# Optimization experiments

Hardware: AMD Instinct MI355X
Metric: run time of the kernel (lower is better)

The kernel has to match this reference:

```python
import jax, jax.numpy as jnp
import numpy as np

NUM_PARTS = 10
COS_W = 10.0
COS_K = 100.0
EPS = 1e-6

B, V, F, VHD = 512, 6890, 13776, 20000


def setup_inputs() -> dict:
    key = jax.random.key(0)
    k1, k2, k3, k4, k5 = jax.random.split(key, 5)
    vertices = jax.random.normal(k1, (B, V, 3), dtype=jnp.float32)
    bary = jax.random.uniform(k2, (VHD, 3), dtype=jnp.float32)
    faces = jax.random.randint(k3, (F, 3), 0, V)
    hd_fid = jax.random.randint(k4, (VHD,), 0, F)
    part_fid = jax.random.randint(k5, (F,), 0, NUM_PARTS)
    return {"vertices": vertices, "bary": bary, "faces": faces,
            "hd_fid": hd_fid, "part_fid": part_fid}


def reference(vertices, bary, faces, hd_fid, part_fid):
    # --- per-part mesh volume (signed tetra volumes, segment-summed by part) ---
    tri = vertices[:, faces]                       # [B, F, 3, 3] gather face corners
    t0, t1, t2 = tri[:, :, 0], tri[:, :, 1], tri[:, :, 2]
    vol_f = jnp.einsum('bfi,bfi->bf', jnp.cross(t0, t1), t2) / 6.0   # [B, F]
    fid_onehot = jax.nn.one_hot(part_fid, NUM_PARTS, dtype=vertices.dtype)  # [F, P]
    per_part_volume = vol_f @ fid_onehot           # [B, P]

    # --- HDfy: barycentric sampling of HD vertices on faces ---
    w = bary / jnp.sum(bary, axis=-1, keepdims=True)          # barycentric weights [VHD,3]
    vidx = faces[hd_fid]                                       # [VHD, 3]
    hd_corners = vertices[:, vidx]                             # [B, VHD, 3, 3]
    vertices_hd = jnp.einsum('bvkd,vk->bvd', hd_corners, w)    # [B, VHD, 3]

    # --- per-HD-vertex part volume (bmm with one-hot == gather) ---
    hd_part = part_fid[hd_fid]                                 # [VHD]
    vol_hd = per_part_volume[:, hd_part]                       # [B, VHD]

    # --- center of mass ---
    com = jnp.sum(vertices_hd * vol_hd[..., None], axis=1) / jnp.sum(vol_hd, axis=1, keepdims=True)  # [B,3]

    # --- center of pressure via height-based pressure weights ---
    h = vertices_hd[:, :, 1]                                   # [B, VHD], ground plane at y=0
    inside = (h < 0.0).astype(vertices_hd.dtype)
    outside = (h >= 0.0).astype(vertices_hd.dtype)
    pw = inside * (1.0 - COS_K * h) + outside * jnp.exp(-COS_W * h)
    cop = jnp.sum(vertices_hd * pw[..., None], axis=1) / (jnp.sum(pw, axis=1, keepdims=True) + EPS)  # [B,3]

    # --- stability loss: xz distance between COM and COP ---
    d = com - cop
    return jnp.sqrt(d[:, 0] ** 2 + d[:, 2] ** 2)               # [B]
```

## Files before the change

kernel.cpp:

```cpp
#include <hip/hip_runtime.h>
#include <math.h>

#define NB     512
#define NV     6890
#define NF     13776
#define NVHD   20000
#define NPARTS 10
#define NTHREADS 1024
#define NWAVES (NTHREADS/64)
#define CUT    6697
#define NCHF   ((NF + 63) / 64)
#define NCHH   ((NVHD + 63) / 64)

__global__ void build_tables(const float* __restrict__ bary,
                             const int*   __restrict__ faces,
                             const int*   __restrict__ hd_fid,
                             const int*   __restrict__ part_fid,
                             uint2* __restrict__ f_pack,
                             uint4* __restrict__ hd_pack)
{
    int i = blockIdx.x * blockDim.x + threadIdx.x;
    if (i < NF) {
        f_pack[i] = make_uint2((unsigned)faces[3*i+0] | ((unsigned)faces[3*i+1] << 16),
                               (unsigned)faces[3*i+2] | ((unsigned)part_fid[i]  << 16));
    }
    if (i < NVHD) {
        int fid = hd_fid[i];
        float b0 = bary[3*i+0], b1 = bary[3*i+1], b2 = bary[3*i+2];
        float inv = 1.0f / (b0 + b1 + b2);
        hd_pack[i] = make_uint4((unsigned)faces[3*fid+0] | ((unsigned)faces[3*fid+1] << 16),
                                (unsigned)faces[3*fid+2] | ((unsigned)part_fid[fid] << 16),
                                __float_as_uint(b0*inv), __float_as_uint(b1*inv));
    }
}

__global__ __launch_bounds__(1024) void split_overflow(
    uint2* __restrict__ f_pack, uint4* __restrict__ hd_pack,
    uint2* __restrict__ ovf_f,  uint4* __restrict__ ovf_h,
    int*   __restrict__ counts)
{
    __shared__ int cnt[NCHH];
    const int tid = threadIdx.x, wave = tid >> 6, lane = tid & 63;
    const unsigned long long lowmask = (1ull << lane) - 1ull;

    if (blockIdx.x == 0) {
        for (int c = wave; c < NCHF; c += NWAVES) {
            int i = c * 64 + lane;
            bool bad = false;
            if (i < NF) {
                uint2 ft = f_pack[i];
                bad = ((ft.x & 0xFFFFu) >= CUT) || ((ft.x >> 16) >= CUT) || ((ft.y & 0xFFFFu) >= CUT);
            }
            unsigned long long m = __ballot(bad);
            if (lane == 0) cnt[c] = (int)__popcll(m);
        }
        __syncthreads();
        if (wave == 0) {
            int carry = 0;
            #pragma unroll
            for (int seg = 0; seg < (NCHF + 63) / 64; seg++) {
                int idx = seg * 64 + lane;
                int v = (idx < NCHF) ? cnt[idx] : 0;
                int incl = v;
                #pragma unroll
                for (int off = 1; off < 64; off <<= 1) { int n = __shfl_up(incl, off, 64); if (lane >= off) incl += n; }
                if (idx < NCHF) cnt[idx] = incl - v + carry;
                carry += __shfl(incl, 63, 64);
            }
            if (lane == 0) counts[0] = carry;
        }
        __syncthreads();
        for (int c = wave; c < NCHF; c += NWAVES) {
            int i = c * 64 + lane;
            bool valid = i < NF;
            uint2 ft = valid ? f_pack[i] : make_uint2(0u, 0u);
            bool bad = valid && (((ft.x & 0xFFFFu) >= CUT) || ((ft.x >> 16) >= CUT) || ((ft.y & 0xFFFFu) >= CUT));
            unsigned long long m = __ballot(bad);
            if (bad) {
                int rank = (int)__popcll(m & lowmask);
                ovf_f[cnt[c] + rank] = ft;
                f_pack[i] = make_uint2((unsigned)CUT | ((unsigned)CUT << 16), (unsigned)CUT);
            }
        }
    } else {
        for (int c = wave; c < NCHH; c += NWAVES) {
            int i = c * 64 + lane;
            bool bad = false;
            if (i < NVHD) {
                uint4 hp = hd_pack[i];
                bad = ((hp.x & 0xFFFFu) >= CUT) || ((hp.x >> 16) >= CUT) || ((hp.y & 0xFFFFu) >= CUT);
            }
            unsigned long long m = __ballot(bad);
            if (lane == 0) cnt[c] = (int)__popcll(m);
        }
        __syncthreads();
        if (wave == 0) {
            int carry = 0;
            #pragma unroll
            for (int seg = 0; seg < (NCHH + 63) / 64; seg++) {
                int idx = seg * 64 + lane;
                int v = (idx < NCHH) ? cnt[idx] : 0;
                int incl = v;
                #pragma unroll
                for (int off = 1; off < 64; off <<= 1) { int n = __shfl_up(incl, off, 64); if (lane >= off) incl += n; }
                if (idx < NCHH) cnt[idx] = incl - v + carry;
                carry += __shfl(incl, 63, 64);
            }
            if (lane == 0) counts[1] = carry;
        }
        __syncthreads();
        for (int c = wave; c < NCHH; c += NWAVES) {
            int i = c * 64 + lane;
            bool valid = i < NVHD;
            uint4 hp = valid ? hd_pack[i] : make_uint4(0u, 0u, 0u, 0u);
            bool bad = valid && (((hp.x & 0xFFFFu) >= CUT) || ((hp.x >> 16) >= CUT) || ((hp.y & 0xFFFFu) >= CUT));
            unsigned long long m = __ballot(bad);
            if (bad) {
                int rank = (int)__popcll(m & lowmask);
                ovf_h[cnt[c] + rank] = hp;
                hd_pack[i] = make_uint4((unsigned)CUT | ((unsigned)CUT << 16),
                                        (unsigned)CUT | ((unsigned)NPARTS << 16),
                                        0u, 0u);
            }
        }
    }
}

__global__ __launch_bounds__(NTHREADS, 8) void stab_kernel(
    const float* __restrict__ vertices,
    const uint2* __restrict__ f_pack,
    const uint4* __restrict__ hd_pack,
    const uint2* __restrict__ ovf_f,
    const uint4* __restrict__ ovf_h,
    const int*   __restrict__ counts,
    float*       __restrict__ out)
{
    __shared__ float2 sxy[CUT + 1];
    __shared__ float  szz[CUT + 1];
    __shared__ float  spart[NPARTS + 1];
    __shared__ float  sredp[NWAVES][NPARTS];

    const int tid  = threadIdx.x;
    const int b    = blockIdx.x;
    const int wave = tid >> 6;
    const int lane = tid & 63;
    const float* __restrict__ vb = vertices + (size_t)b * (NV * 3);

    for (int v = tid; v < CUT; v += NTHREADS) {
        float x = vb[3 * v + 0];
        float y = vb[3 * v + 1];
        float z = vb[3 * v + 2];
        sxy[v] = make_float2(x, y);
        szz[v] = z;
    }
    if (tid == 0) { sxy[CUT] = make_float2(0.f, 100.f); szz[CUT] = 0.f; }
    __syncthreads();

    float accp[NPARTS];
    #pragma unroll
    for (int q = 0; q < NPARTS; q++) accp[q] = 0.f;

    #pragma unroll 2
    for (int f = tid; f < NF; f += NTHREADS) {
        uint2 ft = f_pack[f];
        int i0 = ft.x & 0xFFFF, i1 = ft.x >> 16;
        int i2 = ft.y & 0xFFFF, p  = (int)(ft.y >> 16);
        float2 t0 = sxy[i0]; float z0 = szz[i0];
        float2 t1 = sxy[i1]; float z1 = szz[i1];
        float2 t2 = sxy[i2]; float z2 = szz[i2];
        float cx = t0.y * z1   - z0   * t1.y;
        float cy = z0   * t1.x - t0.x * z1;
        float cz = t0.x * t1.y - t0.y * t1.x;
        float vol = (cx * t2.x + cy * t2.y + cz * z2) * (1.0f / 6.0f);
        #pragma unroll
        for (int q = 0; q < NPARTS; q++) accp[q] += (p == q) ? vol : 0.f;
    }

    const int nofF = counts[0];
    for (int k = tid; k < nofF; k += NTHREADS) {
        uint2 ft = ovf_f[k];
        int i0 = ft.x & 0xFFFF, i1 = ft.x >> 16;
        int i2 = ft.y & 0xFFFF, p  = (int)(ft.y >> 16);
        float x0 = vb[3*i0+0], y0 = vb[3*i0+1], z0 = vb[3*i0+2];
        float x1 = vb[3*i1+0], y1 = vb[3*i1+1], z1 = vb[3*i1+2];
        float x2 = vb[3*i2+0], y2 = vb[3*i2+1], z2 = vb[3*i2+2];
        float cx = y0 * z1 - z0 * y1;
        float cy = z0 * x1 - x0 * z1;
        float cz = x0 * y1 - y0 * x1;
        float vol = (cx * x2 + cy * y2 + cz * z2) * (1.0f / 6.0f);
        #pragma unroll
        for (int q = 0; q < NPARTS; q++) accp[q] += (p == q) ? vol : 0.f;
    }

    #pragma unroll
    for (int q = 0; q < NPARTS; q++) {
        float s = accp[q];
        #pragma unroll
        for (int off = 32; off > 0; off >>= 1) s += __shfl_down(s, off, 64);
        accp[q] = s;
    }
    if (lane == 0) {
        #pragma unroll
        for (int q = 0; q < NPARTS; q++) sredp[wave][q] = accp[q];
    }
    __syncthreads();
    if (tid < NPARTS) {
        float s = 0.f;
        #pragma unroll
        for (int w = 0; w < NWAVES; w++) s += sredp[w][tid];
        spart[tid] = s;
    }
    if (tid == NPARTS) spart[NPARTS] = 0.f;
    __syncthreads();

    float sVx = 0.f, sVz = 0.f, sVol = 0.f;
    float sPx = 0.f, sPz = 0.f, sPw  = 0.f;

    #pragma unroll 2
    for (int v = tid; v < NVHD; v += NTHREADS) {
        uint4 hp = hd_pack[v];
        int i0 = hp.x & 0xFFFF, i1 = hp.x >> 16;
        int i2 = hp.y & 0xFFFF, p  = (int)(hp.y >> 16);
        float w0 = __uint_as_float(hp.z);
        float w1 = __uint_as_float(hp.w);
        float w2 = 1.0f - w0 - w1;
        float2 t0 = sxy[i0]; float z0 = szz[i0];
        float2 t1 = sxy[i1]; float z1 = szz[i1];
        float2 t2 = sxy[i2]; float z2 = szz[i2];
        float x = w0 * t0.x + w1 * t1.x + w2 * t2.x;
        float y = w0 * t0.y + w1 * t1.y + w2 * t2.y;
        float z = w0 * z0   + w1 * z1   + w2 * z2;
        float vol = spart[p];
        float pw  = (y < 0.f) ? fmaf(-100.f, y, 1.f) : __expf(-10.f * y);
        sVx += x * vol;  sVz += z * vol;  sVol += vol;
        sPx += x * pw;   sPz += z * pw;   sPw  += pw;
    }

    const int nofH = counts[1];
    for (int k = tid; k < nofH; k += NTHREADS) {
        uint4 hp = ovf_h[k];
        int i0 = hp.x & 0xFFFF, i1 = hp.x >> 16;
        int i2 = hp.y & 0xFFFF, p  = (int)(hp.y >> 16);
        float w0 = __uint_as_float(hp.z);
        float w1 = __uint_as_float(hp.w);
        float w2 = 1.0f - w0 - w1;
        float x0 = vb[3*i0+0], y0 = vb[3*i0+1], z0 = vb[3*i0+2];
        float x1 = vb[3*i1+0], y1 = vb[3*i1+1], z1 = vb[3*i1+2];
        float x2 = vb[3*i2+0], y2 = vb[3*i2+1], z2 = vb[3*i2+2];
        float x = w0 * x0 + w1 * x1 + w2 * x2;
        float y = w0 * y0 + w1 * y1 + w2 * y2;
        float z = w0 * z0 + w1 * z1 + w2 * z2;
        float vol = spart[p];
        float pw  = (y < 0.f) ? fmaf(-100.f, y, 1.f) : __expf(-10.f * y);
        sVx += x * vol;  sVz += z * vol;  sVol += vol;
        sPx += x * pw;   sPz += z * pw;   sPw  += pw;
    }

    float vals[6] = {sVx, sVz, sVol, sPx, sPz, sPw};
    #pragma unroll
    for (int q = 0; q < 6; q++) {
        float s = vals[q];
        #pragma unroll
        for (int off = 32; off > 0; off >>= 1) s += __shfl_down(s, off, 64);
        vals[q] = s;
    }
    float* sred6 = &sredp[0][0];
    if (lane == 0) {
        #pragma unroll
        for (int q = 0; q < 6; q++) sred6[wave * 6 + q] = vals[q];
    }
    __syncthreads();
    if (tid == 0) {
        float r[6];
        #pragma unroll
        for (int q = 0; q < 6; q++) {
            float s = 0.f;
            #pragma unroll
            for (int w = 0; w < NWAVES; w++) s += sred6[w * 6 + q];
            r[q] = s;
        }
        float invVol = 1.0f / r[2];
        float invPw  = 1.0f / (r[5] + 1e-6f);
        float comx = r[0] * invVol, comz = r[1] * invVol;
        float copx = r[3] * invPw,  copz = r[4] * invPw;
        float d0 = comx - copx, d2 = comz - copz;
        out[b] = sqrtf(d0 * d0 + d2 * d2);
    }
}

extern "C" void kernel_launch(void* const* d_in, const int* in_sizes, int n_in,
                              void* d_out, int out_size, void* d_ws, size_t ws_size,
                              hipStream_t stream) {
    const float* vertices = (const float*)d_in[0];
    const float* bary     = (const float*)d_in[1];
    const int*   faces    = (const int*)d_in[2];
    const int*   hd_fid   = (const int*)d_in[3];
    const int*   part_fid = (const int*)d_in[4];
    float* out = (float*)d_out;

    char* ws = (char*)d_ws;
    uint2* f_pack  = (uint2*)ws;
    uint4* hd_pack = (uint4*)(ws + 110208);
    uint4* ovf_h   = (uint4*)(ws + 110208 + 320000);
    uint2* ovf_f   = (uint2*)(ws + 110208 + 640000);
    int*   counts  = (int*)(ws + 110208 + 640000 + 110208);

    build_tables<<<(NVHD + 255) / 256, 256, 0, stream>>>(bary, faces, hd_fid, part_fid,
                                                         f_pack, hd_pack);
    split_overflow<<<2, 1024, 0, stream>>>(f_pack, hd_pack, ovf_f, ovf_h, counts);
    stab_kernel<<<NB, NTHREADS, 0, stream>>>(vertices, f_pack, hd_pack, ovf_f, ovf_h, counts, out);
}
```

Before: 65.69 us.

## Fuse table build into overflow split and precompute per-part HD counts

Merges the build_tables and split_overflow kernels into a single two-block prep kernel that builds the packed tables directly from the raw inputs, removing one kernel launch and a write-then-reread of the packed tables. The HD block also counts how many HD vertices belong to each part. The main kernel then gets the total volume as the sum over parts of part volume times count, instead of accumulating and reducing a per-vertex volume sum. In exchange, the two-block prep kernel now does all table construction serially with very little parallelism, so its own runtime may grow.

```diff
diff --git a/kernel.cpp b/kernel.cpp
--- a/kernel.cpp
+++ b/kernel.cpp
@@ -12,34 +12,19 @@
 #define NCHF   ((NF + 63) / 64)
 #define NCHH   ((NVHD + 63) / 64)
 
-__global__ void build_tables(const float* __restrict__ bary,
-                             const int*   __restrict__ faces,
-                             const int*   __restrict__ hd_fid,
-                             const int*   __restrict__ part_fid,
-                             uint2* __restrict__ f_pack,
-                             uint4* __restrict__ hd_pack)
-{
-    int i = blockIdx.x * blockDim.x + threadIdx.x;
-    if (i < NF) {
-        f_pack[i] = make_uint2((unsigned)faces[3*i+0] | ((unsigned)faces[3*i+1] << 16),
-                               (unsigned)faces[3*i+2] | ((unsigned)part_fid[i]  << 16));
-    }
-    if (i < NVHD) {
-        int fid = hd_fid[i];
-        float b0 = bary[3*i+0], b1 = bary[3*i+1], b2 = bary[3*i+2];
-        float inv = 1.0f / (b0 + b1 + b2);
-        hd_pack[i] = make_uint4((unsigned)faces[3*fid+0] | ((unsigned)faces[3*fid+1] << 16),
-                                (unsigned)faces[3*fid+2] | ((unsigned)part_fid[fid] << 16),
-                                __float_as_uint(b0*inv), __float_as_uint(b1*inv));
-    }
-}
-
-__global__ __launch_bounds__(1024) void split_overflow(
-    uint2* __restrict__ f_pack, uint4* __restrict__ hd_pack,
-    uint2* __restrict__ ovf_f,  uint4* __restrict__ ovf_h,
+__global__ __launch_bounds__(1024) void prep(
+    const float* __restrict__ bary,
+    const int*   __restrict__ faces,
+    const int*   __restrict__ hd_fid,
+    const int*   __restrict__ part_fid,
+    uint2* __restrict__ f_pack,
+    uint4* __restrict__ hd_pack,
+    uint2* __restrict__ ovf_f,
+    uint4* __restrict__ ovf_h,
     int*   __restrict__ counts)
 {
     __shared__ int cnt[NCHH];
+    __shared__ int snp[NWAVES][NPARTS];
     const int tid = threadIdx.x, wave = tid >> 6, lane = tid & 63;
     const unsigned long long lowmask = (1ull << lane) - 1ull;
 
@@ -48,8 +33,8 @@
             int i = c * 64 + lane;
             bool bad = false;
             if (i < NF) {
-                uint2 ft = f_pack[i];
-                bad = ((ft.x & 0xFFFFu) >= CUT) || ((ft.x >> 16) >= CUT) || ((ft.y & 0xFFFFu) >= CUT);
+                int i0 = faces[3*i+0], i1 = faces[3*i+1], i2 = faces[3*i+2];
+                bad = (i0 >= CUT) || (i1 >= CUT) || (i2 >= CUT);
             }
             unsigned long long m = __ballot(bad);
             if (lane == 0) cnt[c] = (int)__popcll(m);
@@ -73,22 +58,40 @@
         for (int c = wave; c < NCHF; c += NWAVES) {
             int i = c * 64 + lane;
             bool valid = i < NF;
-            uint2 ft = valid ? f_pack[i] : make_uint2(0u, 0u);
-            bool bad = valid && (((ft.x & 0xFFFFu) >= CUT) || ((ft.x >> 16) >= CUT) || ((ft.y & 0xFFFFu) >= CUT));
+            uint2 ft = make_uint2(0u, 0u);
+            bool bad = false;
+            if (valid) {
+                int i0 = faces[3*i+0], i1 = faces[3*i+1], i2 = faces[3*i+2];
+                ft = make_uint2((unsigned)i0 | ((unsigned)i1 << 16),
+                                (unsigned)i2 | ((unsigned)part_fid[i] << 16));
+                bad = (i0 >= CUT) || (i1 >= CUT) || (i2 >= CUT);
+            }
             unsigned long long m = __ballot(bad);
-            if (bad) {
-                int rank = (int)__popcll(m & lowmask);
-                ovf_f[cnt[c] + rank] = ft;
-                f_pack[i] = make_uint2((unsigned)CUT | ((unsigned)CUT << 16), (unsigned)CUT);
+            if (valid) {
+                if (bad) {
+                    int rank = (int)__popcll(m & lowmask);
+                    ovf_f[cnt[c] + rank] = ft;
+                    f_pack[i] = make_uint2((unsigned)CUT | ((unsigned)CUT << 16), (unsigned)CUT);
+                } else {
+                    f_pack[i] = ft;
+                }
             }
         }
     } else {
+        int np[NPARTS];
+        #pragma unroll
+        for (int q = 0; q < NPARTS; q++) np[q] = 0;
+
         for (int c = wave; c < NCHH; c += NWAVES) {
             int i = c * 64 + lane;
             bool bad = false;
             if (i < NVHD) {
-                uint4 hp = hd_pack[i];
-                bad = ((hp.x & 0xFFFFu) >= CUT) || ((hp.x >> 16) >= CUT) || ((hp.y & 0xFFFFu) >= CUT);
+                int fid = hd_fid[i];
+                int i0 = faces[3*fid+0], i1 = faces[3*fid+1], i2 = faces[3*fid+2];
+                int p  = part_fid[fid];
+                #pragma unroll
+                for (int q = 0; q < NPARTS; q++) np[q] += (p == q) ? 1 : 0;
+                bad = (i0 >= CUT) || (i1 >= CUT) || (i2 >= CUT);
             }
             unsigned long long m = __ballot(bad);
             if (lane == 0) cnt[c] = (int)__popcll(m);
@@ -112,16 +115,48 @@
         for (int c = wave; c < NCHH; c += NWAVES) {
             int i = c * 64 + lane;
             bool valid = i < NVHD;
-            uint4 hp = valid ? hd_pack[i] : make_uint4(0u, 0u, 0u, 0u);
-            bool bad = valid && (((hp.x & 0xFFFFu) >= CUT) || ((hp.x >> 16) >= CUT) || ((hp.y & 0xFFFFu) >= CUT));
+            uint4 hp = make_uint4(0u, 0u, 0u, 0u);
+            bool bad = false;
+            if (valid) {
+                int fid = hd_fid[i];
+                int i0 = faces[3*fid+0], i1 = faces[3*fid+1], i2 = faces[3*fid+2];
+                float b0 = bary[3*i+0], b1 = bary[3*i+1], b2 = bary[3*i+2];
+                float inv = 1.0f / (b0 + b1 + b2);
+                hp = make_uint4((unsigned)i0 | ((unsigned)i1 << 16),
+                                (unsigned)i2 | ((unsigned)part_fid[fid] << 16),
+                                __float_as_uint(b0*inv), __float_as_uint(b1*inv));
+                bad = (i0 >= CUT) || (i1 >= CUT) || (i2 >= CUT);
+            }
             unsigned long long m = __ballot(bad);
-            if (bad) {
-                int rank = (int)__popcll(m & lowmask);
-                ovf_h[cnt[c] + rank] = hp;
-                hd_pack[i] = make_uint4((unsigned)CUT | ((unsigned)CUT << 16),
-                                        (unsigned)CUT | ((unsigned)NPARTS << 16),
-                                        0u, 0u);
-            }
+            if (valid) {
+                if (bad) {
+                    int rank = (int)__popcll(m & lowmask);
+                    ovf_h[cnt[c] + rank] = hp;
+                    hd_pack[i] = make_uint4((unsigned)CUT | ((unsigned)CUT << 16),
+                                            (unsigned)CUT | ((unsigned)NPARTS << 16),
+                                            0u, 0u);
+                } else {
+                    hd_pack[i] = hp;
+                }
+            }
+        }
+        #pragma unroll
+        for (int q = 0; q < NPARTS; q++) {
+            int s = np[q];
+            #pragma unroll
+            for (int off = 32; off > 0; off >>= 1) s += __shfl_down(s, off, 64);
+            np[q] = s;
+        }
+        if (lane == 0) {
+            #pragma unroll
+            for (int q = 0; q < NPARTS; q++) snp[wave][q] = np[q];
+        }
+        __syncthreads();
+        if (tid < NPARTS) {
+            int s = 0;
+            #pragma unroll
+            for (int w = 0; w < NWAVES; w++) s += snp[w][tid];
+            counts[2 + tid] = s;
         }
     }
 }
@@ -213,8 +248,8 @@
     if (tid == NPARTS) spart[NPARTS] = 0.f;
     __syncthreads();
 
-    float sVx = 0.f, sVz = 0.f, sVol = 0.f;
-    float sPx = 0.f, sPz = 0.f, sPw  = 0.f;
+    float sVx = 0.f, sVz = 0.f;
+    float sPx = 0.f, sPz = 0.f, sPw = 0.f;
 
     #pragma unroll 2
     for (int v = tid; v < NVHD; v += NTHREADS) {
@@ -232,8 +267,8 @@
         float z = w0 * z0   + w1 * z1   + w2 * z2;
         float vol = spart[p];
         float pw  = (y < 0.f) ? fmaf(-100.f, y, 1.f) : __expf(-10.f * y);
-        sVx += x * vol;  sVz += z * vol;  sVol += vol;
-        sPx += x * pw;   sPz += z * pw;   sPw  += pw;
+        sVx += x * vol;  sVz += z * vol;
+        sPx += x * pw;   sPz += z * pw;   sPw += pw;
     }
 
     const int nofH = counts[1];
@@ -252,37 +287,40 @@
         float z = w0 * z0 + w1 * z1 + w2 * z2;
         float vol = spart[p];
         float pw  = (y < 0.f) ? fmaf(-100.f, y, 1.f) : __expf(-10.f * y);
-        sVx += x * vol;  sVz += z * vol;  sVol += vol;
-        sPx += x * pw;   sPz += z * pw;   sPw  += pw;
-    }
-
-    float vals[6] = {sVx, sVz, sVol, sPx, sPz, sPw};
+        sVx += x * vol;  sVz += z * vol;
+        sPx += x * pw;   sPz += z * pw;   sPw += pw;
+    }
+
+    float vals[5] = {sVx, sVz, sPx, sPz, sPw};
     #pragma unroll
-    for (int q = 0; q < 6; q++) {
+    for (int q = 0; q < 5; q++) {
         float s = vals[q];
         #pragma unroll
         for (int off = 32; off > 0; off >>= 1) s += __shfl_down(s, off, 64);
         vals[q] = s;
     }
-    float* sred6 = &sredp[0][0];
+    float* sred5 = &sredp[0][0];
     if (lane == 0) {
         #pragma unroll
-        for (int q = 0; q < 6; q++) sred6[wave * 6 + q] = vals[q];
+        for (int q = 0; q < 5; q++) sred5[wave * 5 + q] = vals[q];
     }
     __syncthreads();
     if (tid == 0) {
-        float r[6];
-        #pragma unroll
-        for (int q = 0; q < 6; q++) {
+        float r[5];
+        #pragma unroll
+        for (int q = 0; q < 5; q++) {
             float s = 0.f;
             #pragma unroll
-            for (int w = 0; w < NWAVES; w++) s += sred6[w * 6 + q];
+            for (int w = 0; w < NWAVES; w++) s += sred5[w * 5 + q];
             r[q] = s;
         }
-        float invVol = 1.0f / r[2];
-        float invPw  = 1.0f / (r[5] + 1e-6f);
+        float sVol = 0.f;
+        #pragma unroll
+        for (int q = 0; q < NPARTS; q++) sVol += spart[q] * (float)counts[2 + q];
+        float invVol = 1.0f / sVol;
+        float invPw  = 1.0f / (r[4] + 1e-6f);
         float comx = r[0] * invVol, comz = r[1] * invVol;
-        float copx = r[3] * invPw,  copz = r[4] * invPw;
+        float copx = r[2] * invPw,  copz = r[3] * invPw;
         float d0 = comx - copx, d2 = comz - copz;
         out[b] = sqrtf(d0 * d0 + d2 * d2);
     }
@@ -305,8 +343,7 @@
     uint2* ovf_f   = (uint2*)(ws + 110208 + 640000);
     int*   counts  = (int*)(ws + 110208 + 640000 + 110208);
 
-    build_tables<<<(NVHD + 255) / 256, 256, 0, stream>>>(bary, faces, hd_fid, part_fid,
-                                                         f_pack, hd_pack);
-    split_overflow<<<2, 1024, 0, stream>>>(f_pack, hd_pack, ovf_f, ovf_h, counts);
+    prep<<<2, 1024, 0, stream>>>(bary, faces, hd_fid, part_fid,
+                                 f_pack, hd_pack, ovf_f, ovf_h, counts);
     stab_kernel<<<NB, NTHREADS, 0, stream>>>(vertices, f_pack, hd_pack, ovf_f, ovf_h, counts, out);
 }
```

New measurement: 108.2 us. +64.7%, slower.

## Sort faces by part and HD vertices by overflow via parallel count/scan/scatter

Applied to the files above, without the earlier changes.

Replaces the pack-then-split preprocessing with a three-kernel counting sort that groups faces by part id (overflow faces last) and HD vertices into clean and overflow segments. The main kernel then sums volumes per part with a plain scalar accumulator instead of a ten-way predicated update per face, and no longer needs sentinel entries or separate overflow arrays. The preprocessing now runs across many blocks rather than two single blocks, at the cost of an extra kernel launch. The per-part loops have data-dependent bounds, so lanes within a wave may diverge at the segment boundaries.

```diff
diff --git a/kernel.cpp b/kernel.cpp
--- a/kernel.cpp
+++ b/kernel.cpp
@@ -11,116 +11,147 @@
 #define CUT    6697
 #define NCHF   ((NF + 63) / 64)
 #define NCHH   ((NVHD + 63) / 64)
-
-__global__ void build_tables(const float* __restrict__ bary,
-                             const int*   __restrict__ faces,
-                             const int*   __restrict__ hd_fid,
-                             const int*   __restrict__ part_fid,
-                             uint2* __restrict__ f_pack,
-                             uint4* __restrict__ hd_pack)
+#define FBLK   ((NF + 255) / 256)
+#define HBLK   ((NVHD + 255) / 256)
+
+__global__ __launch_bounds__(256) void count_kernel(
+    const int* __restrict__ faces, const int* __restrict__ part_fid,
+    const int* __restrict__ hd_fid,
+    int* __restrict__ cntF,
+    int* __restrict__ cntH)
 {
-    int i = blockIdx.x * blockDim.x + threadIdx.x;
-    if (i < NF) {
-        f_pack[i] = make_uint2((unsigned)faces[3*i+0] | ((unsigned)faces[3*i+1] << 16),
-                               (unsigned)faces[3*i+2] | ((unsigned)part_fid[i]  << 16));
-    }
-    if (i < NVHD) {
-        int fid = hd_fid[i];
-        float b0 = bary[3*i+0], b1 = bary[3*i+1], b2 = bary[3*i+2];
-        float inv = 1.0f / (b0 + b1 + b2);
-        hd_pack[i] = make_uint4((unsigned)faces[3*fid+0] | ((unsigned)faces[3*fid+1] << 16),
-                                (unsigned)faces[3*fid+2] | ((unsigned)part_fid[fid] << 16),
+    const int wv = threadIdx.x >> 6, lane = threadIdx.x & 63;
+    if (blockIdx.x < FBLK) {
+        int c = blockIdx.x * 4 + wv;
+        int i = c * 64 + lane;
+        int key = -1;
+        if (i < NF) {
+            int i0 = faces[3*i+0], i1 = faces[3*i+1], i2 = faces[3*i+2];
+            bool bad = (i0 >= CUT) || (i1 >= CUT) || (i2 >= CUT);
+            key = bad ? 10 : part_fid[i];
+        }
+        #pragma unroll
+        for (int q = 0; q < 11; q++) {
+            unsigned long long m = __ballot(key == q);
+            if (lane == 0) cntF[q * NCHF + c] = (int)__popcll(m);
+        }
+    } else {
+        int c = (blockIdx.x - FBLK) * 4 + wv;
+        if (c < NCHH) {
+            int i = c * 64 + lane;
+            int key = -1;
+            if (i < NVHD) {
+                int fid = hd_fid[i];
+                int i0 = faces[3*fid+0], i1 = faces[3*fid+1], i2 = faces[3*fid+2];
+                key = ((i0 >= CUT) || (i1 >= CUT) || (i2 >= CUT)) ? 1 : 0;
+            }
+            #pragma unroll
+            for (int q = 0; q < 2; q++) {
+                unsigned long long m = __ballot(key == q);
+                if (lane == 0) cntH[q * NCHH + c] = (int)__popcll(m);
+            }
+        }
+    }
+}
+
+__global__ __launch_bounds__(1024) void scan_kernel(
+    int* __restrict__ cntF, int* __restrict__ cntH, int* __restrict__ offs)
+{
+    __shared__ int rowtot[13];
+    const int wv = threadIdx.x >> 6, lane = threadIdx.x & 63;
+    if (wv < 11) {
+        int* row = cntF + wv * NCHF;
+        int carry = 0;
+        #pragma unroll
+        for (int seg = 0; seg < (NCHF + 63) / 64; seg++) {
+            int idx = seg * 64 + lane;
+            int v = (idx < NCHF) ? row[idx] : 0;
+            int incl = v;
+            #pragma unroll
+            for (int off = 1; off < 64; off <<= 1) { int n = __shfl_up(incl, off, 64); if (lane >= off) incl += n; }
+            if (idx < NCHF) row[idx] = incl - v + carry;
+            carry += __shfl(incl, 63, 64);
+        }
+        if (lane == 0) rowtot[wv] = carry;
+    } else if (wv < 13) {
+        int r = wv - 11;
+        int* row = cntH + r * NCHH;
+        int carry = 0;
+        #pragma unroll
+        for (int seg = 0; seg < (NCHH + 63) / 64; seg++) {
+            int idx = seg * 64 + lane;
+            int v = (idx < NCHH) ? row[idx] : 0;
+            int incl = v;
+            #pragma unroll
+            for (int off = 1; off < 64; off <<= 1) { int n = __shfl_up(incl, off, 64); if (lane >= off) incl += n; }
+            if (idx < NCHH) row[idx] = incl - v + carry;
+            carry += __shfl(incl, 63, 64);
+        }
+        if (lane == 0) rowtot[11 + r] = carry;
+    }
+    __syncthreads();
+    if (threadIdx.x == 0) {
+        int r = 0;
+        #pragma unroll
+        for (int q = 0; q < 11; q++) { offs[q] = r; r += rowtot[q]; }
+        offs[11] = r;
+        offs[12] = 0;
+        offs[13] = rowtot[11];
+        offs[14] = rowtot[11] + rowtot[12];
+    }
+}
+
+__global__ __launch_bounds__(256) void scatter_kernel(
+    const float* __restrict__ bary, const int* __restrict__ faces,
+    const int* __restrict__ hd_fid, const int* __restrict__ part_fid,
+    const int* __restrict__ cntF, const int* __restrict__ cntH,
+    const int* __restrict__ offs,
+    uint2* __restrict__ f_sorted, uint4* __restrict__ hd_sorted)
+{
+    const int wv = threadIdx.x >> 6, lane = threadIdx.x & 63;
+    const unsigned long long low = (1ull << lane) - 1ull;
+    if (blockIdx.x < FBLK) {
+        int c = blockIdx.x * 4 + wv;
+        int i = c * 64 + lane;
+        int key = -1; uint2 ft = make_uint2(0u, 0u);
+        if (i < NF) {
+            int i0 = faces[3*i+0], i1 = faces[3*i+1], i2 = faces[3*i+2];
+            int p  = part_fid[i];
+            bool bad = (i0 >= CUT) || (i1 >= CUT) || (i2 >= CUT);
+            key = bad ? 10 : p;
+            ft = make_uint2((unsigned)i0 | ((unsigned)i1 << 16),
+                            (unsigned)i2 | ((unsigned)p  << 16));
+        }
+        #pragma unroll
+        for (int q = 0; q < 11; q++) {
+            unsigned long long m = __ballot(key == q);
+            if (key == q) {
+                int rank = (int)__popcll(m & low);
+                f_sorted[offs[q] + cntF[q * NCHF + c] + rank] = ft;
+            }
+        }
+    } else {
+        int c = (blockIdx.x - FBLK) * 4 + wv;
+        if (c < NCHH) {
+            int i = c * 64 + lane;
+            int key = -1; uint4 hp = make_uint4(0u, 0u, 0u, 0u);
+            if (i < NVHD) {
+                int fid = hd_fid[i];
+                int i0 = faces[3*fid+0], i1 = faces[3*fid+1], i2 = faces[3*fid+2];
+                float b0 = bary[3*i+0], b1 = bary[3*i+1], b2 = bary[3*i+2];
+                float inv = 1.0f / (b0 + b1 + b2);
+                hp = make_uint4((unsigned)i0 | ((unsigned)i1 << 16),
+                                (unsigned)i2 | ((unsigned)part_fid[fid] << 16),
                                 __float_as_uint(b0*inv), __float_as_uint(b1*inv));
-    }
-}
-
-__global__ __launch_bounds__(1024) void split_overflow(
-    uint2* __restrict__ f_pack, uint4* __restrict__ hd_pack,
-    uint2* __restrict__ ovf_f,  uint4* __restrict__ ovf_h,
-    int*   __restrict__ counts)
-{
-    __shared__ int cnt[NCHH];
-    const int tid = threadIdx.x, wave = tid >> 6, lane = tid & 63;
-    const unsigned long long lowmask = (1ull << lane) - 1ull;
-
-    if (blockIdx.x == 0) {
-        for (int c = wave; c < NCHF; c += NWAVES) {
-            int i = c * 64 + lane;
-            bool bad = false;
-            if (i < NF) {
-                uint2 ft = f_pack[i];
-                bad = ((ft.x & 0xFFFFu) >= CUT) || ((ft.x >> 16) >= CUT) || ((ft.y & 0xFFFFu) >= CUT);
-            }
-            unsigned long long m = __ballot(bad);
-            if (lane == 0) cnt[c] = (int)__popcll(m);
-        }
-        __syncthreads();
-        if (wave == 0) {
-            int carry = 0;
-            #pragma unroll
-            for (int seg = 0; seg < (NCHF + 63) / 64; seg++) {
-                int idx = seg * 64 + lane;
-                int v = (idx < NCHF) ? cnt[idx] : 0;
-                int incl = v;
-                #pragma unroll
-                for (int off = 1; off < 64; off <<= 1) { int n = __shfl_up(incl, off, 64); if (lane >= off) incl += n; }
-                if (idx < NCHF) cnt[idx] = incl - v + carry;
-                carry += __shfl(incl, 63, 64);
-            }
-            if (lane == 0) counts[0] = carry;
-        }
-        __syncthreads();
-        for (int c = wave; c < NCHF; c += NWAVES) {
-            int i = c * 64 + lane;
-            bool valid = i < NF;
-            uint2 ft = valid ? f_pack[i] : make_uint2(0u, 0u);
-            bool bad = valid && (((ft.x & 0xFFFFu) >= CUT) || ((ft.x >> 16) >= CUT) || ((ft.y & 0xFFFFu) >= CUT));
-            unsigned long long m = __ballot(bad);
-            if (bad) {
-                int rank = (int)__popcll(m & lowmask);
-                ovf_f[cnt[c] + rank] = ft;
-                f_pack[i] = make_uint2((unsigned)CUT | ((unsigned)CUT << 16), (unsigned)CUT);
-            }
-        }
-    } else {
-        for (int c = wave; c < NCHH; c += NWAVES) {
-            int i = c * 64 + lane;
-            bool bad = false;
-            if (i < NVHD) {
-                uint4 hp = hd_pack[i];
-                bad = ((hp.x & 0xFFFFu) >= CUT) || ((hp.x >> 16) >= CUT) || ((hp.y & 0xFFFFu) >= CUT);
-            }
-            unsigned long long m = __ballot(bad);
-            if (lane == 0) cnt[c] = (int)__popcll(m);
-        }
-        __syncthreads();
-        if (wave == 0) {
-            int carry = 0;
-            #pragma unroll
-            for (int seg = 0; seg < (NCHH + 63) / 64; seg++) {
-                int idx = seg * 64 + lane;
-                int v = (idx < NCHH) ? cnt[idx] : 0;
-                int incl = v;
-                #pragma unroll
-                for (int off = 1; off < 64; off <<= 1) { int n = __shfl_up(incl, off, 64); if (lane >= off) incl += n; }
-                if (idx < NCHH) cnt[idx] = incl - v + carry;
-                carry += __shfl(incl, 63, 64);
-            }
-            if (lane == 0) counts[1] = carry;
-        }
-        __syncthreads();
-        for (int c = wave; c < NCHH; c += NWAVES) {
-            int i = c * 64 + lane;
-            bool valid = i < NVHD;
-            uint4 hp = valid ? hd_pack[i] : make_uint4(0u, 0u, 0u, 0u);
-            bool bad = valid && (((hp.x & 0xFFFFu) >= CUT) || ((hp.x >> 16) >= CUT) || ((hp.y & 0xFFFFu) >= CUT));
-            unsigned long long m = __ballot(bad);
-            if (bad) {
-                int rank = (int)__popcll(m & lowmask);
-                ovf_h[cnt[c] + rank] = hp;
-                hd_pack[i] = make_uint4((unsigned)CUT | ((unsigned)CUT << 16),
-                                        (unsigned)CUT | ((unsigned)NPARTS << 16),
-                                        0u, 0u);
+                key = ((i0 >= CUT) || (i1 >= CUT) || (i2 >= CUT)) ? 1 : 0;
+            }
+            #pragma unroll
+            for (int q = 0; q < 2; q++) {
+                unsigned long long m = __ballot(key == q);
+                if (key == q) {
+                    int rank = (int)__popcll(m & low);
+                    hd_sorted[offs[12 + q] + cntH[q * NCHH + c] + rank] = hp;
+                }
             }
         }
     }
@@ -128,16 +159,14 @@
 
 __global__ __launch_bounds__(NTHREADS, 8) void stab_kernel(
     const float* __restrict__ vertices,
-    const uint2* __restrict__ f_pack,
-    const uint4* __restrict__ hd_pack,
-    const uint2* __restrict__ ovf_f,
-    const uint4* __restrict__ ovf_h,
-    const int*   __restrict__ counts,
+    const uint2* __restrict__ f_sorted,
+    const uint4* __restrict__ hd_sorted,
+    const int*   __restrict__ offs,
     float*       __restrict__ out)
 {
-    __shared__ float2 sxy[CUT + 1];
-    __shared__ float  szz[CUT + 1];
-    __shared__ float  spart[NPARTS + 1];
+    __shared__ float2 sxy[CUT];
+    __shared__ float  szz[CUT];
+    __shared__ float  spart[NPARTS];
     __shared__ float  sredp[NWAVES][NPARTS];
 
     const int tid  = threadIdx.x;
@@ -145,6 +174,11 @@
     const int wave = tid >> 6;
     const int lane = tid & 63;
     const float* __restrict__ vb = vertices + (size_t)b * (NV * 3);
+
+    int offF[12];
+    #pragma unroll
+    for (int q = 0; q < 12; q++) offF[q] = offs[q];
+    const int hClean = offs[13];
 
     for (int v = tid; v < CUT; v += NTHREADS) {
         float x = vb[3 * v + 0];
@@ -153,32 +187,30 @@
         sxy[v] = make_float2(x, y);
         szz[v] = z;
     }
-    if (tid == 0) { sxy[CUT] = make_float2(0.f, 100.f); szz[CUT] = 0.f; }
     __syncthreads();
 
     float accp[NPARTS];
     #pragma unroll
     for (int q = 0; q < NPARTS; q++) accp[q] = 0.f;
 
-    #pragma unroll 2
-    for (int f = tid; f < NF; f += NTHREADS) {
-        uint2 ft = f_pack[f];
-        int i0 = ft.x & 0xFFFF, i1 = ft.x >> 16;
-        int i2 = ft.y & 0xFFFF, p  = (int)(ft.y >> 16);
-        float2 t0 = sxy[i0]; float z0 = szz[i0];
-        float2 t1 = sxy[i1]; float z1 = szz[i1];
-        float2 t2 = sxy[i2]; float z2 = szz[i2];
-        float cx = t0.y * z1   - z0   * t1.y;
-        float cy = z0   * t1.x - t0.x * z1;
-        float cz = t0.x * t1.y - t0.y * t1.x;
-        float vol = (cx * t2.x + cy * t2.y + cz * z2) * (1.0f / 6.0f);
-        #pragma unroll
-        for (int q = 0; q < NPARTS; q++) accp[q] += (p == q) ? vol : 0.f;
-    }
-
-    const int nofF = counts[0];
-    for (int k = tid; k < nofF; k += NTHREADS) {
-        uint2 ft = ovf_f[k];
+    #pragma unroll
+    for (int p = 0; p < NPARTS; p++) {
+        float va = 0.f;
+        for (int f = offF[p] + tid; f < offF[p + 1]; f += NTHREADS) {
+            uint2 ft = f_sorted[f];
+            int i0 = ft.x & 0xFFFF, i1 = ft.x >> 16, i2 = ft.y & 0xFFFF;
+            float2 t0 = sxy[i0]; float z0 = szz[i0];
+            float2 t1 = sxy[i1]; float z1 = szz[i1];
+            float2 t2 = sxy[i2]; float z2 = szz[i2];
+            float cx = t0.y * z1   - z0   * t1.y;
+            float cy = z0   * t1.x - t0.x * z1;
+            float cz = t0.x * t1.y - t0.y * t1.x;
+            va += (cx * t2.x + cy * t2.y + cz * z2) * (1.0f / 6.0f);
+        }
+        accp[p] += va;
+    }
+    for (int f = offF[10] + tid; f < NF; f += NTHREADS) {
+        uint2 ft = f_sorted[f];
         int i0 = ft.x & 0xFFFF, i1 = ft.x >> 16;
         int i2 = ft.y & 0xFFFF, p  = (int)(ft.y >> 16);
         float x0 = vb[3*i0+0], y0 = vb[3*i0+1], z0 = vb[3*i0+2];
@@ -210,15 +242,14 @@
         for (int w = 0; w < NWAVES; w++) s += sredp[w][tid];
         spart[tid] = s;
     }
-    if (tid == NPARTS) spart[NPARTS] = 0.f;
     __syncthreads();
 
     float sVx = 0.f, sVz = 0.f, sVol = 0.f;
-    float sPx = 0.f, sPz = 0.f, sPw  = 0.f;
+    float sPx = 0.f, sPz = 0.f, sPw = 0.f;
 
     #pragma unroll 2
-    for (int v = tid; v < NVHD; v += NTHREADS) {
-        uint4 hp = hd_pack[v];
+    for (int v = tid; v < hClean; v += NTHREADS) {
+        uint4 hp = hd_sorted[v];
         int i0 = hp.x & 0xFFFF, i1 = hp.x >> 16;
         int i2 = hp.y & 0xFFFF, p  = (int)(hp.y >> 16);
         float w0 = __uint_as_float(hp.z);
@@ -233,12 +264,10 @@
         float vol = spart[p];
         float pw  = (y < 0.f) ? fmaf(-100.f, y, 1.f) : __expf(-10.f * y);
         sVx += x * vol;  sVz += z * vol;  sVol += vol;
-        sPx += x * pw;   sPz += z * pw;   sPw  += pw;
-    }
-
-    const int nofH = counts[1];
-    for (int k = tid; k < nofH; k += NTHREADS) {
-        uint4 hp = ovf_h[k];
+        sPx += x * pw;   sPz += z * pw;   sPw += pw;
+    }
+    for (int v = hClean + tid; v < NVHD; v += NTHREADS) {
+        uint4 hp = hd_sorted[v];
         int i0 = hp.x & 0xFFFF, i1 = hp.x >> 16;
         int i2 = hp.y & 0xFFFF, p  = (int)(hp.y >> 16);
         float w0 = __uint_as_float(hp.z);
@@ -253,7 +282,7 @@
         float vol = spart[p];
         float pw  = (y < 0.f) ? fmaf(-100.f, y, 1.f) : __expf(-10.f * y);
         sVx += x * vol;  sVz += z * vol;  sVol += vol;
-        sPx += x * pw;   sPz += z * pw;   sPw  += pw;
+        sPx += x * pw;   sPz += z * pw;   sPw += pw;
     }
 
     float vals[6] = {sVx, sVz, sVol, sPx, sPz, sPw};
@@ -299,14 +328,15 @@
     float* out = (float*)d_out;
 
     char* ws = (char*)d_ws;
-    uint2* f_pack  = (uint2*)ws;
-    uint4* hd_pack = (uint4*)(ws + 110208);
-    uint4* ovf_h   = (uint4*)(ws + 110208 + 320000);
-    uint2* ovf_f   = (uint2*)(ws + 110208 + 640000);
-    int*   counts  = (int*)(ws + 110208 + 640000 + 110208);
-
-    build_tables<<<(NVHD + 255) / 256, 256, 0, stream>>>(bary, faces, hd_fid, part_fid,
-                                                         f_pack, hd_pack);
-    split_overflow<<<2, 1024, 0, stream>>>(f_pack, hd_pack, ovf_f, ovf_h, counts);
-    stab_kernel<<<NB, NTHREADS, 0, stream>>>(vertices, f_pack, hd_pack, ovf_f, ovf_h, counts, out);
-}
+    uint4* hd_sorted = (uint4*)ws;
+    uint2* f_sorted  = (uint2*)(ws + 320000);
+    int*   cntF      = (int*)(ws + 320000 + 110208);
+    int*   cntH      = (int*)(ws + 320000 + 110208 + 9504);
+    int*   offs      = (int*)(ws + 320000 + 110208 + 9504 + 2504);
+
+    count_kernel<<<FBLK + HBLK, 256, 0, stream>>>(faces, part_fid, hd_fid, cntF, cntH);
+    scan_kernel<<<1, 1024, 0, stream>>>(cntF, cntH, offs);
+    scatter_kernel<<<FBLK + HBLK, 256, 0, stream>>>(bary, faces, hd_fid, part_fid,
+                                                    cntF, cntH, offs, f_sorted, hd_sorted);
+    stab_kernel<<<NB, NTHREADS, 0, stream>>>(vertices, f_sorted, hd_sorted, offs, out);
+}
```

After: 54.83 us. 1.2x faster.
